# Optimization experiments

Measured on AMD Instinct MI355X. Metric: run time of the kernel, lower is better.

## Reference

```python
import jax, jax.numpy as jnp
import numpy as np

B, C, Ci, V = 1024, 256, 128, 90
EPS = 1e-5


def setup_inputs() -> dict:
    key = jax.random.key(0)
    ks = iter(jax.random.split(key, 40))
    def nrm(shape, s=1.0):
        return jax.random.normal(next(ks), shape, jnp.float32) * s
    def uni(shape):
        return jax.random.uniform(next(ks), shape, jnp.float32, 0.5, 1.5)
    inp = {"x1": nrm((B, C, V)), "x2": nrm((B, C, V))}
    for p in ["g", "th", "ph"]:
        inp[p + "_bn_gamma"] = uni((C,))
        inp[p + "_bn_beta"] = nrm((C,), 0.1)
        inp[p + "_bn_mean"] = nrm((C,), 0.1)
        inp[p + "_bn_var"] = uni((C,))
        inp[p + "_w"] = nrm((Ci, C), 0.05)
        inp[p + "_b"] = nrm((Ci,), 0.05)
    inp["W_w"] = nrm((C, Ci), 0.05)
    inp["W_b"] = nrm((C,), 0.05)
    inp["W_bn_gamma"] = uni((C,))
    inp["W_bn_beta"] = nrm((C,), 0.1)
    inp["W_bn_mean"] = nrm((C,), 0.1)
    inp["W_bn_var"] = uni((C,))
    inp["qt_w"] = nrm((Ci, C), 0.05); inp["qt_b"] = nrm((Ci,), 0.05)
    inp["ks_w"] = nrm((Ci, V), 0.05); inp["ks_b"] = nrm((Ci,), 0.05)
    inp["qs_w"] = nrm((Ci, V), 0.05); inp["qs_b"] = nrm((Ci,), 0.05)
    inp["kt_w"] = nrm((Ci, C), 0.05); inp["kt_b"] = nrm((Ci,), 0.05)
    return inp


def _bn(x, g, b, m, v):
    # eval-mode BatchNorm1d over channel dim of (B, C, V)
    return (x - m[:, None]) * jax.lax.rsqrt(v[:, None] + EPS) * g[:, None] + b[:, None]


def _conv1(x, w, b):
    # 1x1 Conv1d: (B, Cin, V) x (Cout, Cin) -> (B, Cout, V)
    return jnp.einsum('bcv,oc->bov', x, w) + b[:, None]


def reference(x1, x2,
              g_bn_gamma, g_bn_beta, g_bn_mean, g_bn_var, g_w, g_b,
              th_bn_gamma, th_bn_beta, th_bn_mean, th_bn_var, th_w, th_b,
              ph_bn_gamma, ph_bn_beta, ph_bn_mean, ph_bn_var, ph_w, ph_b,
              W_w, W_b, W_bn_gamma, W_bn_beta, W_bn_mean, W_bn_var,
              qt_w, qt_b, ks_w, ks_b, qs_w, qs_b, kt_w, kt_b):
    g_x1 = _conv1(_bn(x1, g_bn_gamma, g_bn_beta, g_bn_mean, g_bn_var), g_w, g_b)
    g_x2 = _conv1(_bn(x2, g_bn_gamma, g_bn_beta, g_bn_mean, g_bn_var), g_w, g_b)
    theta = _conv1(_bn(x1, th_bn_gamma, th_bn_beta, th_bn_mean, th_bn_var), th_w, th_b)  # theta(x1)
    phi = _conv1(_bn(x2, ph_bn_gamma, ph_bn_beta, ph_bn_mean, ph_bn_var), ph_w, ph_b)    # phi(x2)

    e_time = jnp.einsum('biv,bjv->bij', theta, phi)   # (B, Ci, Ci) = theta_x1 @ phi_x2
    e_space = jnp.einsum('bci,bcj->bij', theta, phi)  # (B, V, V)  = theta_x2 @ phi_x1

    attn_time_1 = jax.nn.softmax(e_time, axis=-1)
    attn_time_2 = jax.nn.softmax(jnp.swapaxes(e_time, 1, 2), axis=-1)
    attn_space_2 = jax.nn.softmax(e_space, axis=-1)
    attn_space_1 = jax.nn.softmax(jnp.swapaxes(e_space, 1, 2), axis=-1)

    z1 = jnp.einsum('bij,bjv,bvw->biw', attn_time_2, g_x1, attn_space_2)  # (B, Ci, V)
    z2 = jnp.einsum('bij,bjv,bvw->biw', attn_time_1, g_x2, attn_space_1)

    m1t = x1.mean(axis=2)                      # (B, C)
    q_time = m1t @ qt_w.T + qt_b               # (B, Ci)
    k_space = x2.mean(axis=1) @ ks_w.T + ks_b  # (B, Ci)
    # bmm of (B,1,Ci) x (B,Ci,1) -> (B,1,1); softmax over singleton dim == 1 (kept for faithfulness)
    attn_t2s = jax.nn.softmax(jnp.sum(q_time * k_space, axis=-1, keepdims=True)[:, :, None], axis=-1)
    x2n = x2 + attn_t2s * m1t[:, :, None]      # broadcast (B,1,1)*(B,C,1) over V

    q_space = x1.mean(axis=1) @ qs_w.T + qs_b  # (B, Ci)
    k_time = x2n.mean(axis=2) @ kt_w.T + kt_b  # (B, Ci)
    attn_s2t = jax.nn.softmax(jnp.sum(q_space * k_time, axis=-1, keepdims=True)[:, :, None], axis=-1)
    x1n = x1 + attn_s2t * x2n.mean(axis=1)[:, None, :]

    def Wop(z):
        return _bn(_conv1(z, W_w, W_b), W_bn_gamma, W_bn_beta, W_bn_mean, W_bn_var)

    return (x1n + Wop(z1), x2n + Wop(z2))
```

## Files before the change

### kernel.cpp

```cpp
#include <hip/hip_runtime.h>

namespace {

constexpr int B = 1024;

using u16 = unsigned short;
using u32 = unsigned int;

typedef __attribute__((ext_vector_type(8))) short bf16x8;
typedef __attribute__((ext_vector_type(4))) float f32x4;

#define MFMA16(a, b, c) __builtin_amdgcn_mfma_f32_16x16x32_bf16(a, b, c, 0, 0, 0)

__device__ __forceinline__ u16 f2bf(float f) {
  u32 u = __builtin_bit_cast(u32, f);
  u += 0x7FFFu + ((u >> 16) & 1u);
  return (u16)(u >> 16);
}
__device__ __forceinline__ float bf2f(u16 s) {
  u32 u = ((u32)s) << 16;
  return __builtin_bit_cast(float, u);
}
__device__ __forceinline__ u32 packbf2(float a, float b) {
  return (u32)f2bf(a) | ((u32)f2bf(b) << 16);
}
__device__ __forceinline__ u32 tsplit(float f) {
  u32 u = __builtin_bit_cast(u32, f);
  float r = f - __builtin_bit_cast(float, u & 0xFFFF0000u);
  u32 ur = __builtin_bit_cast(u32, r);
  return (u >> 16) | (ur & 0xFFFF0000u);
}

__global__ __launch_bounds__(256) void k0_fold(
    const float* __restrict__ gg, const float* __restrict__ gbe, const float* __restrict__ gme, const float* __restrict__ gva,
    const float* __restrict__ gw, const float* __restrict__ gbi,
    const float* __restrict__ tg, const float* __restrict__ tbe, const float* __restrict__ tme, const float* __restrict__ tva,
    const float* __restrict__ tw, const float* __restrict__ tbi,
    const float* __restrict__ pg, const float* __restrict__ pbe, const float* __restrict__ pme, const float* __restrict__ pva,
    const float* __restrict__ pw, const float* __restrict__ pbi,
    const float* __restrict__ Ww, const float* __restrict__ Wb,
    const float* __restrict__ Wg2, const float* __restrict__ Wbe, const float* __restrict__ Wme, const float* __restrict__ Wva,
    u16* __restrict__ wgo, float* __restrict__ bgo,
    u16* __restrict__ wthi, u16* __restrict__ wtlo, float* __restrict__ bto,
    u16* __restrict__ wphi, u16* __restrict__ wplo, float* __restrict__ bpo,
    u16* __restrict__ wWo, float* __restrict__ bWo)
{
  __shared__ float red[4];
  const int blk = blockIdx.x, tid = threadIdx.x;
  if (blk < 384) {
    const int p = blk >> 7, o = blk & 127;
    const float *ga, *be, *me, *va, *wm, *bi;
    if (p == 0)      { ga = gg; be = gbe; me = gme; va = gva; wm = gw; bi = gbi; }
    else if (p == 1) { ga = tg; be = tbe; me = tme; va = tva; wm = tw; bi = tbi; }
    else             { ga = pg; be = pbe; me = pme; va = pva; wm = pw; bi = pbi; }
    float s = ga[tid] * rsqrtf(va[tid] + 1e-5f);
    float t = be[tid] - me[tid] * s;
    float wv = wm[o * 256 + tid];
    float val = wv * s;
    if (p == 0) {
      wgo[o * 256 + tid] = f2bf(val);
    } else {
      u16 hi = f2bf(val);
      u16 lo = f2bf(val - bf2f(hi));
      if (p == 1) { wthi[o * 256 + tid] = hi; wtlo[o * 256 + tid] = lo; }
      else        { wphi[o * 256 + tid] = hi; wplo[o * 256 + tid] = lo; }
    }
    float part = t * wv;
#pragma unroll
    for (int off = 32; off; off >>= 1) part += __shfl_down(part, off);
    if ((tid & 63) == 0) red[tid >> 6] = part;
    __syncthreads();
    if (tid == 0) {
      float bsum = bi[o] + red[0] + red[1] + red[2] + red[3];
      if (p == 0) bgo[o] = bsum; else if (p == 1) bto[o] = bsum; else bpo[o] = bsum;
    }
  } else {
    const int c = blk - 384;
    float sW = Wg2[c] * rsqrtf(Wva[c] + 1e-5f);
    if (tid < 128) wWo[c * 128 + tid] = f2bf(Ww[c * 128 + tid] * sW);
    if (tid == 0) bWo[c] = Wb[c] * sW + Wbe[c] - Wme[c] * sW;
  }
}

__global__ __launch_bounds__(512, 4) void k1_conv(
    const float* __restrict__ x1, const float* __restrict__ x2,
    const u16* __restrict__ wG, const float* __restrict__ bG,
    const u16* __restrict__ wTh, const u16* __restrict__ wTl, const float* __restrict__ bT,
    const u16* __restrict__ wPh, const u16* __restrict__ wPl, const float* __restrict__ bP,
    u32* __restrict__ thRm, u32* __restrict__ phRm,
    u16* __restrict__ outU,
    float* __restrict__ m1t, float* __restrict__ x2cm, float* __restrict__ x1am)
{
  __shared__ u32 qb[64 * 92];
  __shared__ u16 xh[96 * 136];
  __shared__ u16 xl[96 * 136];
  __shared__ float red[4];
  const int bid = blockIdx.x, tid = threadIdx.x;
  const int b = bid >> 1; const bool isX1 = !(bid & 1);
  const int l = tid & 63, wv = tid >> 6, lr = l & 15, lq = l >> 4;
  const f32x4 zero = {0.f, 0.f, 0.f, 0.f};

  const float* xb = (isX1 ? x1 : x2) + (size_t)b * 23040;
  const u16* Wh = isX1 ? wTh : wPh;
  const u16* Wl = isX1 ? wTl : wPl;
  const float* biasT = isX1 ? bT : bP;
  u16* oSl = outU + (size_t)(isX1 ? b : 1024 + b) * 46080;
  u32* rmDst = (isX1 ? thRm : phRm) + (size_t)b * 12288;
  u32* pkDst = (u32*)(oSl + 12288);
  u16* gDst = oSl;

  f32x4 aT[6], aG[6];
#pragma unroll
  for (int i = 0; i < 6; ++i) { aT[i] = zero; aG[i] = zero; }
  float cs = 0.f;

  for (int h = 0; h < 2; ++h) {
    for (int q = 0; q < 2; ++q) {
      __syncthreads();
      const float* src = xb + (2 * h + q) * 5760;
      for (int t = tid; t < 2880; t += 512) {
        float2 f = *(const float2*)(src + 2 * t);
        int cl = (2 * t) / 90, v = 2 * t - 90 * cl;
        uint2 w; w.x = tsplit(f.x); w.y = tsplit(f.y);
        *(uint2*)&qb[cl * 92 + v] = w;
      }
      __syncthreads();
      for (int t = tid; t < 1440; t += 512) {
        int v = t % 90, c4 = t / 90;
        u32 p0 = qb[(4 * c4 + 0) * 92 + v], p1 = qb[(4 * c4 + 1) * 92 + v];
        u32 p2 = qb[(4 * c4 + 2) * 92 + v], p3 = qb[(4 * c4 + 3) * 92 + v];
        uint2 hi, lo;
        hi.x = (p0 & 0xFFFFu) | (p1 << 16);
        hi.y = (p2 & 0xFFFFu) | (p3 << 16);
        lo.x = (p0 >> 16) | (p1 & 0xFFFF0000u);
        lo.y = (p2 >> 16) | (p3 & 0xFFFF0000u);
        int base = v * 136 + 64 * q + 4 * c4;
        *(uint2*)&xh[base] = hi;
        *(uint2*)&xl[base] = lo;
      }
      if (q == 1) {
        for (int t = tid; t < 384; t += 512) {
          int v = 90 + (t >> 6), c2 = (t & 63) * 2;
          *(u32*)&xh[v * 136 + c2] = 0u;
          *(u32*)&xl[v * 136 + c2] = 0u;
        }
      }
      if (!isX1 && tid < 90) {
        float s = 0.f;
        for (int cl = 0; cl < 64; ++cl) {
          u32 p = qb[cl * 92 + tid];
          s += bf2f((u16)p) + bf2f((u16)(p >> 16));
        }
        cs += s;
      }
    }
    __syncthreads();
    if (isX1 && tid < 128) {
      float s = 0.f;
      for (int v = 0; v < 90; ++v) s += bf2f(xh[v * 136 + tid]) + bf2f(xl[v * 136 + tid]);
      m1t[b * 256 + 128 * h + tid] = s * (1.f / 90.f);
#pragma unroll
      for (int o = 32; o; o >>= 1) s += __shfl_down(s, o);
      if ((tid & 63) == 0) red[(tid >> 6) + 2 * h] = s;
    }
    for (int kk = 0; kk < 4; ++kk) {
      const int wo = (16 * wv + lr) * 256 + 128 * h + kk * 32 + 8 * lq;
      bf16x8 ah = *(const bf16x8*)(Wh + wo);
      bf16x8 al = *(const bf16x8*)(Wl + wo);
      bf16x8 ag = *(const bf16x8*)(wG + wo);
#pragma unroll
      for (int nt = 0; nt < 6; ++nt) {
        const int bo = (16 * nt + lr) * 136 + kk * 32 + 8 * lq;
        bf16x8 bh = *(const bf16x8*)&xh[bo];
        bf16x8 bl = *(const bf16x8*)&xl[bo];
        aT[nt] = MFMA16(ah, bh, aT[nt]);
        aT[nt] = MFMA16(ah, bl, aT[nt]);
        aT[nt] = MFMA16(al, bh, aT[nt]);
        aG[nt] = MFMA16(ag, bh, aG[nt]);
        aG[nt] = MFMA16(ag, bl, aG[nt]);
      }
    }
  }
  __syncthreads();
  const int c0 = 16 * wv + 4 * lq;
  const float4 bt4 = *(const float4*)(biasT + c0);
  const float4 bg4 = *(const float4*)(bG + c0);
#pragma unroll
  for (int nt = 0; nt < 6; ++nt) {
    const int v = 16 * nt + lr;
    u32 pk0, pk1, pk2, pk3; uint2 gpk;
    if (v < 90) {
      pk0 = tsplit(aT[nt][0] + bt4.x);
      pk1 = tsplit(aT[nt][1] + bt4.y);
      pk2 = tsplit(aT[nt][2] + bt4.z);
      pk3 = tsplit(aT[nt][3] + bt4.w);
      gpk.x = packbf2(aG[nt][0] + bg4.x, aG[nt][1] + bg4.y);
      gpk.y = packbf2(aG[nt][2] + bg4.z, aG[nt][3] + bg4.w);
    } else { pk0 = pk1 = pk2 = pk3 = 0u; gpk.x = 0u; gpk.y = 0u; }
    uint4 q4; q4.x = pk0; q4.y = pk1; q4.z = pk2; q4.w = pk3;
    *(uint4*)(pkDst + v * 128 + c0) = q4;
    rmDst[(c0 + 0) * 96 + v] = pk0;
    rmDst[(c0 + 1) * 96 + v] = pk1;
    rmDst[(c0 + 2) * 96 + v] = pk2;
    rmDst[(c0 + 3) * 96 + v] = pk3;
    *(uint2*)(gDst + v * 128 + c0) = gpk;
  }
  if (isX1) {
    if (tid == 0) x1am[b] = (red[0] + red[1] + red[2] + red[3]) * (1.f / 23040.f);
  } else {
    if (tid < 90) x2cm[b * 96 + tid] = cs * (1.f / 256.f);
  }
}

__global__ __launch_bounds__(512) void k2_attn(
    const u32* __restrict__ thRm, const u32* __restrict__ phRm,
    u16* __restrict__ outU,
    u16* __restrict__ At1g, u16* __restrict__ At2g)
{
  __shared__ __align__(16) char smem[108544];
  u16* s0 = (u16*)smem;
  float* st = (float*)(smem + 106496);
  float* eL = (float*)smem;

  const int bid = blockIdx.x, tid = threadIdx.x;
  const int b = bid >> 1;
  const int l = tid & 63, wv = tid >> 6, lr = l & 15, lq = l >> 4;
  const f32x4 zero = {0.f, 0.f, 0.f, 0.f};

  if (!(bid & 1)) {
    const u32* thRmB = thRm + (size_t)b * 12288;
    const u32* phRmB = phRm + (size_t)b * 12288;
    u16* th_hi = s0;
    u16* th_lo = s0 + 13312;
    u16* ph_hi = s0 + 26624;
    u16* ph_lo = s0 + 39936;
    for (int d = tid; d < 6144; d += 512) {
      int ten = (d >= 3072);
      int i = d - 3072 * ten;
      int ci = i / 24, q4 = i - 24 * ci;
      uint4 P = *(const uint4*)((ten ? phRmB : thRmB) + ci * 96 + 4 * q4);
      uint2 hi, lo;
      hi.x = (P.x & 0xFFFFu) | (P.y << 16);
      hi.y = (P.z & 0xFFFFu) | (P.w << 16);
      lo.x = (P.x >> 16) | (P.y & 0xFFFF0000u);
      lo.y = (P.z >> 16) | (P.w & 0xFFFF0000u);
      *(uint2*)((ten ? ph_hi : th_hi) + ci * 104 + 4 * q4) = hi;
      *(uint2*)((ten ? ph_lo : th_lo) + ci * 104 + 4 * q4) = lo;
    }
    __syncthreads();
    f32x4 acc[8];
#pragma unroll
    for (int nt = 0; nt < 8; ++nt) acc[nt] = zero;
#pragma unroll
    for (int kk = 0; kk < 3; ++kk) {
      const int ao = (16 * wv + lr) * 104 + kk * 32 + 8 * lq;
      bf16x8 ah = *(const bf16x8*)&th_hi[ao];
      bf16x8 al = *(const bf16x8*)&th_lo[ao];
#pragma unroll
      for (int nt = 0; nt < 8; ++nt) {
        const int bo = (16 * nt + lr) * 104 + kk * 32 + 8 * lq;
        bf16x8 bh = *(const bf16x8*)&ph_hi[bo];
        bf16x8 bl = *(const bf16x8*)&ph_lo[bo];
        acc[nt] = MFMA16(ah, bh, acc[nt]);
        acc[nt] = MFMA16(ah, bl, acc[nt]);
        acc[nt] = MFMA16(al, bh, acc[nt]);
      }
    }
    __syncthreads();
#pragma unroll
    for (int nt = 0; nt < 8; ++nt)
#pragma unroll
      for (int r = 0; r < 4; ++r)
        eL[(16 * nt + lr) * 133 + 16 * wv + 4 * lq + r] = acc[nt][r];
    __syncthreads();
    if (tid < 128) {
      int j = tid; float m = -1e30f;
      for (int i = 0; i < 128; ++i) m = fmaxf(m, eL[j * 133 + i]);
      float s = 0.f;
      for (int i = 0; i < 128; ++i) s += __expf(eL[j * 133 + i] - m);
      st[j] = m; st[128 + j] = 1.f / s;
    } else if (tid < 256) {
      int i = tid - 128; float m = -1e30f;
      for (int j = 0; j < 128; ++j) m = fmaxf(m, eL[j * 133 + i]);
      float s = 0.f;
      for (int j = 0; j < 128; ++j) s += __expf(eL[j * 133 + i] - m);
      st[256 + i] = m; st[384 + i] = 1.f / s;
    }
    __syncthreads();
    u32* A1 = (u32*)(At1g + (size_t)b * 16384);
    u32* A2 = (u32*)(At2g + (size_t)b * 16384);
    for (int d = tid; d < 8192; d += 512) {
      int i = d >> 6, jp = d & 63;
      float m1 = st[256 + i], s1v = st[384 + i];
      float a0 = __expf(eL[(2 * jp) * 133 + i] - m1) * s1v;
      float a1 = __expf(eL[(2 * jp + 1) * 133 + i] - m1) * s1v;
      A1[d] = packbf2(a0, a1);
      float m2 = st[i], s2v = st[128 + i];
      float b0 = __expf(eL[i * 133 + 2 * jp] - m2) * s2v;
      float b1 = __expf(eL[i * 133 + 2 * jp + 1] - m2) * s2v;
      A2[d] = packbf2(b0, b1);
    }
    return;
  }

  const u32* thPk = (const u32*)(outU + (size_t)b * 46080 + 12288);
  const u32* phPk = (const u32*)(outU + (size_t)(1024 + b) * 46080 + 12288);
  u32* S1 = (u32*)(outU + (size_t)(1024 + b) * 46080 + 36864);
  u32* S2 = (u32*)(outU + (size_t)b * 46080 + 36864);

  u16* tTh = s0;
  u16* tTl = s0 + 13056;
  u16* pTh = s0 + 26112;
  u16* pTl = s0 + 39168;
  for (int d = tid; d < 6144; d += 512) {
    int ten = (d >= 3072);
    int i = d - 3072 * ten;
    int v = i >> 5, q4 = i & 31;
    uint4 P = *(const uint4*)((ten ? phPk : thPk) + v * 128 + 4 * q4);
    uint2 hi, lo;
    hi.x = (P.x & 0xFFFFu) | (P.y << 16);
    hi.y = (P.z & 0xFFFFu) | (P.w << 16);
    lo.x = (P.x >> 16) | (P.y & 0xFFFF0000u);
    lo.y = (P.z >> 16) | (P.w & 0xFFFF0000u);
    *(uint2*)((ten ? pTh : tTh) + v * 136 + 4 * q4) = hi;
    *(uint2*)((ten ? pTl : tTl) + v * 136 + 4 * q4) = lo;
  }
  __syncthreads();
  f32x4 accS[5];
#pragma unroll
  for (int it = 0; it < 5; ++it) accS[it] = zero;
#pragma unroll
  for (int it = 0; it < 5; ++it) {
    const int t5 = wv + 8 * it;
    if (t5 < 36) {
      const int mt = t5 / 6, nt = t5 - 6 * (t5 / 6);
#pragma unroll
      for (int kk = 0; kk < 4; ++kk) {
        const int ao = (16 * mt + lr) * 136 + kk * 32 + 8 * lq;
        const int bo = (16 * nt + lr) * 136 + kk * 32 + 8 * lq;
        bf16x8 ah = *(const bf16x8*)&tTh[ao];
        bf16x8 al = *(const bf16x8*)&tTl[ao];
        bf16x8 bh = *(const bf16x8*)&pTh[bo];
        bf16x8 bl = *(const bf16x8*)&pTl[bo];
        accS[it] = MFMA16(ah, bh, accS[it]);
        accS[it] = MFMA16(ah, bl, accS[it]);
        accS[it] = MFMA16(al, bh, accS[it]);
      }
    }
  }
  __syncthreads();
  {
    float* esL = (float*)smem;
#pragma unroll
    for (int it = 0; it < 5; ++it) {
      const int t5 = wv + 8 * it;
      if (t5 < 36) {
        const int mt = t5 / 6, nt = t5 - 6 * (t5 / 6);
#pragma unroll
        for (int r = 0; r < 4; ++r)
          esL[(16 * nt + lr) * 101 + 16 * mt + 4 * lq + r] = accS[it][r];
      }
    }
  }
  __syncthreads();
  {
    float* esL = (float*)smem;
    if (tid < 96) {
      int v = tid; float m = -1e30f;
      for (int w2 = 0; w2 < 90; ++w2) m = fmaxf(m, esL[v * 101 + w2]);
      float s = 0.f;
      for (int w2 = 0; w2 < 90; ++w2) s += __expf(esL[v * 101 + w2] - m);
      st[v] = m; st[128 + v] = 1.f / s;
    } else if (tid >= 128 && tid < 224) {
      int v = tid - 128; float m = -1e30f;
      for (int w2 = 0; w2 < 90; ++w2) m = fmaxf(m, esL[w2 * 101 + v]);
      float s = 0.f;
      for (int w2 = 0; w2 < 90; ++w2) s += __expf(esL[w2 * 101 + v] - m);
      st[256 + v] = m; st[384 + v] = 1.f / s;
    }
  }
  __syncthreads();
  {
    float* esL = (float*)smem;
    for (int d = tid; d < 4608; d += 512) {
      int w2 = d / 48, vp = d - 48 * (d / 48);
      int v0 = 2 * vp, v1 = v0 + 1;
      float a0 = __expf(esL[v0 * 101 + w2] - st[v0]) * st[128 + v0];
      float a1 = __expf(esL[v1 * 101 + w2] - st[v1]) * st[128 + v1];
      S1[d] = packbf2(a0, a1);
      float b0 = __expf(esL[w2 * 101 + v0] - st[256 + v0]) * st[384 + v0];
      float b1 = __expf(esL[w2 * 101 + v1] - st[256 + v1]) * st[384 + v1];
      S2[d] = packbf2(b0, b1);
    }
  }
}

__global__ __launch_bounds__(256) void k3_out(
    const float* __restrict__ x1, const float* __restrict__ x2,
    const u16* __restrict__ At1g, const u16* __restrict__ At2g,
    const u16* __restrict__ wW, const float* __restrict__ bW,
    const float* __restrict__ m1t, const float* __restrict__ x2cm, const float* __restrict__ x1am,
    float* __restrict__ out)
{
  __shared__ u16 gT[96 * 136];
  __shared__ u16 Tb[128 * 104];
  __shared__ u16 ZT[96 * 136];
  const int bid = blockIdx.x, tid = threadIdx.x;
  const int b = bid >> 1; const bool modeA = !(bid & 1);
  const int l = tid & 63, wv = tid >> 6, lr = l & 15, lq = l >> 4;
  const f32x4 zero = {0.f, 0.f, 0.f, 0.f};

  float* out1 = out + (size_t)b * 23040;
  float* out2 = out + (size_t)23040 * 1024 + (size_t)b * 23040;

  const u16* gsrc; const u16* At; const u16* AsT; const float* xres; float* dst;
  if (modeA) {
    gsrc = (const u16*)out2; At = At1g + (size_t)b * 16384;
    AsT = (const u16*)out2 + 36864; xres = x2 + (size_t)b * 23040; dst = out2;
  } else {
    gsrc = (const u16*)out1; At = At2g + (size_t)b * 16384;
    AsT = (const u16*)out1 + 36864; xres = x1 + (size_t)b * 23040; dst = out1;
  }

  for (int i = tid; i < 1536; i += 256) {
    int v = i >> 4, hh = i & 15;
    *(uint4*)&gT[v * 136 + 8 * hh] = ((const uint4*)gsrc)[i];
  }
  __syncthreads();
#pragma unroll
  for (int ni = 0; ni < 2; ++ni) {
    const int nt = 2 * wv + ni;
    f32x4 acc[6];
#pragma unroll
    for (int i = 0; i < 6; ++i) acc[i] = zero;
#pragma unroll
    for (int kk = 0; kk < 4; ++kk) {
      bf16x8 bb = *(const bf16x8*)(At + (16 * nt + lr) * 128 + kk * 32 + 8 * lq);
#pragma unroll
      for (int mt = 0; mt < 6; ++mt) {
        bf16x8 a = *(const bf16x8*)&gT[(16 * mt + lr) * 136 + kk * 32 + 8 * lq];
        acc[mt] = MFMA16(a, bb, acc[mt]);
      }
    }
#pragma unroll
    for (int mt = 0; mt < 6; ++mt) {
      uint2 pk;
      pk.x = packbf2(acc[mt][0], acc[mt][1]);
      pk.y = packbf2(acc[mt][2], acc[mt][3]);
      *(uint2*)&Tb[(16 * nt + lr) * 104 + 16 * mt + 4 * lq] = pk;
    }
  }
  __syncthreads();
  {
    f32x4 acc[2][6];
#pragma unroll
    for (int i = 0; i < 2; ++i)
#pragma unroll
      for (int j = 0; j < 6; ++j) acc[i][j] = zero;
#pragma unroll
    for (int kk = 0; kk < 3; ++kk) {
      bf16x8 a0 = *(const bf16x8*)&Tb[(16 * (2 * wv) + lr) * 104 + kk * 32 + 8 * lq];
      bf16x8 a1 = *(const bf16x8*)&Tb[(16 * (2 * wv + 1) + lr) * 104 + kk * 32 + 8 * lq];
#pragma unroll
      for (int nt = 0; nt < 6; ++nt) {
        bf16x8 bb = *(const bf16x8*)(AsT + (16 * nt + lr) * 96 + kk * 32 + 8 * lq);
        acc[0][nt] = MFMA16(a0, bb, acc[0][nt]);
        acc[1][nt] = MFMA16(a1, bb, acc[1][nt]);
      }
    }
#pragma unroll
    for (int mi = 0; mi < 2; ++mi) {
      const int mt = 2 * wv + mi;
#pragma unroll
      for (int nt = 0; nt < 6; ++nt) {
        uint2 pk;
        pk.x = packbf2(acc[mi][nt][0], acc[mi][nt][1]);
        pk.y = packbf2(acc[mi][nt][2], acc[mi][nt][3]);
        *(uint2*)&ZT[(16 * nt + lr) * 136 + 16 * mt + 4 * lq] = pk;
      }
    }
  }
  __syncthreads();
  const float am = modeA ? 0.f : x1am[b];
#pragma unroll
  for (int mi = 0; mi < 4; ++mi) {
    const int mt = 4 * wv + mi;
    f32x4 acc[6];
#pragma unroll
    for (int i = 0; i < 6; ++i) acc[i] = zero;
#pragma unroll
    for (int kk = 0; kk < 4; ++kk) {
      bf16x8 a = *(const bf16x8*)(wW + (16 * mt + lr) * 128 + kk * 32 + 8 * lq);
#pragma unroll
      for (int nt = 0; nt < 6; ++nt) {
        bf16x8 bb = *(const bf16x8*)&ZT[(16 * nt + lr) * 136 + kk * 32 + 8 * lq];
        acc[nt] = MFMA16(a, bb, acc[nt]);
      }
    }
    const int c0 = 16 * mt + 4 * lq;
    const float4 bw4 = *(const float4*)(bW + c0);
    float bwA[4] = {bw4.x, bw4.y, bw4.z, bw4.w};
    float mA[4] = {0.f, 0.f, 0.f, 0.f};
    if (modeA) {
      const float4 m4 = *(const float4*)(m1t + b * 256 + c0);
      mA[0] = m4.x; mA[1] = m4.y; mA[2] = m4.z; mA[3] = m4.w;
    }
#pragma unroll
    for (int nt = 0; nt < 6; ++nt) {
      const int v = 16 * nt + lr;
      if (v < 90) {
        const float addv = modeA ? 0.f : (am + x2cm[b * 96 + v]);
#pragma unroll
        for (int r = 0; r < 4; ++r) {
          const int c = c0 + r;
          const float extra = modeA ? mA[r] : addv;
          dst[c * 90 + v] = xres[c * 90 + v] + acc[nt][r] + bwA[r] + extra;
        }
      }
    }
  }
}

}

extern "C" void kernel_launch(void* const* d_in, const int* in_sizes, int n_in,
                              void* d_out, int out_size, void* d_ws, size_t ws_size,
                              hipStream_t stream)
{
  (void)in_sizes; (void)n_in; (void)out_size; (void)ws_size;
  const float* x1  = (const float*)d_in[0];
  const float* x2  = (const float*)d_in[1];
  const float* gg  = (const float*)d_in[2];
  const float* gbe = (const float*)d_in[3];
  const float* gme = (const float*)d_in[4];
  const float* gva = (const float*)d_in[5];
  const float* gw  = (const float*)d_in[6];
  const float* gbi = (const float*)d_in[7];
  const float* tg  = (const float*)d_in[8];
  const float* tbe = (const float*)d_in[9];
  const float* tme = (const float*)d_in[10];
  const float* tva = (const float*)d_in[11];
  const float* tw  = (const float*)d_in[12];
  const float* tbi = (const float*)d_in[13];
  const float* pg  = (const float*)d_in[14];
  const float* pbe = (const float*)d_in[15];
  const float* pme = (const float*)d_in[16];
  const float* pva = (const float*)d_in[17];
  const float* pw  = (const float*)d_in[18];
  const float* pbi = (const float*)d_in[19];
  const float* Ww  = (const float*)d_in[20];
  const float* Wb  = (const float*)d_in[21];
  const float* Wg  = (const float*)d_in[22];
  const float* Wbe = (const float*)d_in[23];
  const float* Wme = (const float*)d_in[24];
  const float* Wva = (const float*)d_in[25];

  float* out = (float*)d_out;
  unsigned char* W8 = (unsigned char*)d_ws;

  size_t off = 0;
  auto al = [&](size_t n) { size_t r = off; off += (n + 255) & ~(size_t)255; return r; };
  const size_t oWG  = al(65536);
  const size_t oWTh = al(65536), oWTl = al(65536);
  const size_t oWPh = al(65536), oWPl = al(65536);
  const size_t oWW  = al(65536);
  const size_t oBG = al(512), oBT = al(512), oBP = al(512), oBW = al(1024);
  const size_t oRM1 = al((size_t)B * 49152), oRM2 = al((size_t)B * 49152);
  const size_t oA1 = al((size_t)B * 32768), oA2 = al((size_t)B * 32768);
  const size_t oM1 = al((size_t)B * 1024), oXC = al((size_t)B * 384), oXA = al((size_t)B * 4);

  k0_fold<<<dim3(640), dim3(256), 0, stream>>>(
      gg, gbe, gme, gva, gw, gbi,
      tg, tbe, tme, tva, tw, tbi,
      pg, pbe, pme, pva, pw, pbi,
      Ww, Wb, Wg, Wbe, Wme, Wva,
      (u16*)(W8 + oWG), (float*)(W8 + oBG),
      (u16*)(W8 + oWTh), (u16*)(W8 + oWTl), (float*)(W8 + oBT),
      (u16*)(W8 + oWPh), (u16*)(W8 + oWPl), (float*)(W8 + oBP),
      (u16*)(W8 + oWW), (float*)(W8 + oBW));

  k1_conv<<<dim3(2 * B), dim3(512), 0, stream>>>(
      x1, x2,
      (const u16*)(W8 + oWG), (const float*)(W8 + oBG),
      (const u16*)(W8 + oWTh), (const u16*)(W8 + oWTl), (const float*)(W8 + oBT),
      (const u16*)(W8 + oWPh), (const u16*)(W8 + oWPl), (const float*)(W8 + oBP),
      (u32*)(W8 + oRM1), (u32*)(W8 + oRM2),
      (u16*)out,
      (float*)(W8 + oM1), (float*)(W8 + oXC), (float*)(W8 + oXA));

  k2_attn<<<dim3(2 * B), dim3(512), 0, stream>>>(
      (const u32*)(W8 + oRM1), (const u32*)(W8 + oRM2),
      (u16*)out,
      (u16*)(W8 + oA1), (u16*)(W8 + oA2));

  k3_out<<<dim3(2 * B), dim3(256), 0, stream>>>(
      x1, x2,
      (const u16*)(W8 + oA1), (const u16*)(W8 + oA2),
      (const u16*)(W8 + oWW), (const float*)(W8 + oBW),
      (const float*)(W8 + oM1), (const float*)(W8 + oXC), (const float*)(W8 + oXA),
      out);
}
```

Baseline: 521.7 us.

## Widen k3_out to 512 threads, stage As in LDS, coalesce output via LDS

Doubles the k3_out block to 512 threads so each wave owns one tile row instead of two. The spatial attention matrix is prefetched into registers early and then staged into shared memory, so the second GMM reads it from LDS instead of global memory. Final output tiles are transposed through a per-wave LDS buffer and written with contiguous row-major stores, giving coalesced residual reads and output writes. The cost is extra barriers inside the output loop and higher shared-memory use per block, which may limit how many blocks fit on a CU.

New measurement: 576.0 us. +10.4%, slower.

```diff
diff --git a/kernel.cpp b/kernel.cpp
--- a/kernel.cpp
+++ b/kernel.cpp
@@ -395,16 +395,20 @@
   }
 }
 
-__global__ __launch_bounds__(256) void k3_out(
+__global__ __launch_bounds__(512, 4) void k3_out(
     const float* __restrict__ x1, const float* __restrict__ x2,
     const u16* __restrict__ At1g, const u16* __restrict__ At2g,
     const u16* __restrict__ wW, const float* __restrict__ bW,
     const float* __restrict__ m1t, const float* __restrict__ x2cm, const float* __restrict__ x1am,
     float* __restrict__ out)
 {
-  __shared__ u16 gT[96 * 136];
-  __shared__ u16 Tb[128 * 104];
-  __shared__ u16 ZT[96 * 136];
+  __shared__ __align__(16) char smem[78848];
+  u16* gT = (u16*)smem;
+  u16* As = (u16*)smem;
+  u16* Tb = (u16*)(smem + 26112);
+  u16* ZT = (u16*)(smem + 52736);
+  float* OtBase = (float*)smem;
+
   const int bid = blockIdx.x, tid = threadIdx.x;
   const int b = bid >> 1; const bool modeA = !(bid & 1);
   const int l = tid & 63, wv = tid >> 6, lr = l & 15, lq = l >> 4;
@@ -413,29 +417,33 @@
   float* out1 = out + (size_t)b * 23040;
   float* out2 = out + (size_t)23040 * 1024 + (size_t)b * 23040;
 
-  const u16* gsrc; const u16* At; const u16* AsT; const float* xres; float* dst;
+  const u16* gsrc; const u16* At; const u16* AsG; const float* xres; float* dst;
   if (modeA) {
     gsrc = (const u16*)out2; At = At1g + (size_t)b * 16384;
-    AsT = (const u16*)out2 + 36864; xres = x2 + (size_t)b * 23040; dst = out2;
+    AsG = (const u16*)out2 + 36864; xres = x2 + (size_t)b * 23040; dst = out2;
   } else {
     gsrc = (const u16*)out1; At = At2g + (size_t)b * 16384;
-    AsT = (const u16*)out1 + 36864; xres = x1 + (size_t)b * 23040; dst = out1;
-  }
-
-  for (int i = tid; i < 1536; i += 256) {
+    AsG = (const u16*)out1 + 36864; xres = x1 + (size_t)b * 23040; dst = out1;
+  }
+
+  const uint4* As4 = (const uint4*)AsG;
+  uint4 asr0 = As4[tid];
+  uint4 asr1 = As4[512 + tid];
+  uint4 asr2 = {0, 0, 0, 0};
+  if (tid < 128) asr2 = As4[1024 + tid];
+
+  for (int i = tid; i < 1536; i += 512) {
     int v = i >> 4, hh = i & 15;
     *(uint4*)&gT[v * 136 + 8 * hh] = ((const uint4*)gsrc)[i];
   }
   __syncthreads();
-#pragma unroll
-  for (int ni = 0; ni < 2; ++ni) {
-    const int nt = 2 * wv + ni;
+  {
     f32x4 acc[6];
 #pragma unroll
     for (int i = 0; i < 6; ++i) acc[i] = zero;
 #pragma unroll
     for (int kk = 0; kk < 4; ++kk) {
-      bf16x8 bb = *(const bf16x8*)(At + (16 * nt + lr) * 128 + kk * 32 + 8 * lq);
+      bf16x8 bb = *(const bf16x8*)(At + (16 * wv + lr) * 128 + kk * 32 + 8 * lq);
 #pragma unroll
       for (int mt = 0; mt < 6; ++mt) {
         bf16x8 a = *(const bf16x8*)&gT[(16 * mt + lr) * 136 + kk * 32 + 8 * lq];
@@ -447,44 +455,43 @@
       uint2 pk;
       pk.x = packbf2(acc[mt][0], acc[mt][1]);
       pk.y = packbf2(acc[mt][2], acc[mt][3]);
-      *(uint2*)&Tb[(16 * nt + lr) * 104 + 16 * mt + 4 * lq] = pk;
+      *(uint2*)&Tb[(16 * wv + lr) * 104 + 16 * mt + 4 * lq] = pk;
     }
   }
   __syncthreads();
   {
-    f32x4 acc[2][6];
-#pragma unroll
-    for (int i = 0; i < 2; ++i)
-#pragma unroll
-      for (int j = 0; j < 6; ++j) acc[i][j] = zero;
+    int i0 = tid;            *(uint4*)&As[(i0 / 12) * 104 + (i0 % 12) * 8] = asr0;
+    int i1 = 512 + tid;      *(uint4*)&As[(i1 / 12) * 104 + (i1 % 12) * 8] = asr1;
+    if (tid < 128) { int i2 = 1024 + tid; *(uint4*)&As[(i2 / 12) * 104 + (i2 % 12) * 8] = asr2; }
+  }
+  __syncthreads();
+  {
+    f32x4 acc[6];
+#pragma unroll
+    for (int i = 0; i < 6; ++i) acc[i] = zero;
 #pragma unroll
     for (int kk = 0; kk < 3; ++kk) {
-      bf16x8 a0 = *(const bf16x8*)&Tb[(16 * (2 * wv) + lr) * 104 + kk * 32 + 8 * lq];
-      bf16x8 a1 = *(const bf16x8*)&Tb[(16 * (2 * wv + 1) + lr) * 104 + kk * 32 + 8 * lq];
+      bf16x8 a0 = *(const bf16x8*)&Tb[(16 * wv + lr) * 104 + kk * 32 + 8 * lq];
 #pragma unroll
       for (int nt = 0; nt < 6; ++nt) {
-        bf16x8 bb = *(const bf16x8*)(AsT + (16 * nt + lr) * 96 + kk * 32 + 8 * lq);
-        acc[0][nt] = MFMA16(a0, bb, acc[0][nt]);
-        acc[1][nt] = MFMA16(a1, bb, acc[1][nt]);
-      }
-    }
-#pragma unroll
-    for (int mi = 0; mi < 2; ++mi) {
-      const int mt = 2 * wv + mi;
-#pragma unroll
-      for (int nt = 0; nt < 6; ++nt) {
-        uint2 pk;
-        pk.x = packbf2(acc[mi][nt][0], acc[mi][nt][1]);
-        pk.y = packbf2(acc[mi][nt][2], acc[mi][nt][3]);
-        *(uint2*)&ZT[(16 * nt + lr) * 136 + 16 * mt + 4 * lq] = pk;
-      }
+        bf16x8 bb = *(const bf16x8*)&As[(16 * nt + lr) * 104 + kk * 32 + 8 * lq];
+        acc[nt] = MFMA16(a0, bb, acc[nt]);
+      }
+    }
+#pragma unroll
+    for (int nt = 0; nt < 6; ++nt) {
+      uint2 pk;
+      pk.x = packbf2(acc[nt][0], acc[nt][1]);
+      pk.y = packbf2(acc[nt][2], acc[nt][3]);
+      *(uint2*)&ZT[(16 * nt + lr) * 136 + 16 * wv + 4 * lq] = pk;
     }
   }
   __syncthreads();
   const float am = modeA ? 0.f : x1am[b];
-#pragma unroll
-  for (int mi = 0; mi < 4; ++mi) {
-    const int mt = 4 * wv + mi;
+  float* Ot = OtBase + wv * 1472;
+#pragma unroll
+  for (int mi = 0; mi < 2; ++mi) {
+    const int mt = 2 * wv + mi;
     f32x4 acc[6];
 #pragma unroll
     for (int i = 0; i < 6; ++i) acc[i] = zero;
@@ -497,25 +504,26 @@
         acc[nt] = MFMA16(a, bb, acc[nt]);
       }
     }
-    const int c0 = 16 * mt + 4 * lq;
-    const float4 bw4 = *(const float4*)(bW + c0);
-    float bwA[4] = {bw4.x, bw4.y, bw4.z, bw4.w};
-    float mA[4] = {0.f, 0.f, 0.f, 0.f};
-    if (modeA) {
-      const float4 m4 = *(const float4*)(m1t + b * 256 + c0);
-      mA[0] = m4.x; mA[1] = m4.y; mA[2] = m4.z; mA[3] = m4.w;
-    }
+    __syncthreads();
 #pragma unroll
     for (int nt = 0; nt < 6; ++nt) {
       const int v = 16 * nt + lr;
       if (v < 90) {
-        const float addv = modeA ? 0.f : (am + x2cm[b * 96 + v]);
-#pragma unroll
-        for (int r = 0; r < 4; ++r) {
-          const int c = c0 + r;
-          const float extra = modeA ? mA[r] : addv;
-          dst[c * 90 + v] = xres[c * 90 + v] + acc[nt][r] + bwA[r] + extra;
-        }
+#pragma unroll
+        for (int r = 0; r < 4; ++r) Ot[(4 * lq + r) * 92 + v] = acc[nt][r];
+      }
+    }
+    __syncthreads();
+    const int c0b = 16 * mt;
+#pragma unroll 4
+    for (int k = 0; k < 23; ++k) {
+      int f = 64 * k + l;
+      if (f < 1440) {
+        int row = f / 90, col = f - 90 * row;
+        int c = c0b + row;
+        float o = Ot[row * 92 + col];
+        float extra = modeA ? m1t[b * 256 + c] : (am + x2cm[b * 96 + col]);
+        dst[c * 90 + col] = xres[c * 90 + col] + o + bW[c] + extra;
       }
     }
   }
@@ -593,7 +601,7 @@
       (u16*)out,
       (u16*)(W8 + oA1), (u16*)(W8 + oA2));
 
-  k3_out<<<dim3(2 * B), dim3(256), 0, stream>>>(
+  k3_out<<<dim3(2 * B), dim3(512), 0, stream>>>(
       x1, x2,
       (const u16*)(W8 + oA1), (const u16*)(W8 + oA2),
       (const u16*)(W8 + oWW), (const float*)(W8 + oBW),
```

## Merge the two k3_out modes into one block per batch and alias LDS buffers

Applied to the files above, without the earlier changes.

Each block of k3_out now handles both output modes for one batch element, one after the other, so the grid is halved. The gT and ZT staging buffers share one LDS region, which lowers per-block shared memory. Launch bounds now request 3 blocks per SIMD/CU to raise occupancy and hide latency. In exchange, each block does twice the serial work and adds an extra barrier, and with fewer blocks the wave tail on the GPU may get worse.

New measurement: 574.3 us. 1.1x slower.

```diff
diff --git a/kernel.cpp b/kernel.cpp
--- a/kernel.cpp
+++ b/kernel.cpp
@@ -395,130 +395,133 @@
   }
 }
 
-__global__ __launch_bounds__(256) void k3_out(
+__global__ __launch_bounds__(256, 3) void k3_out(
     const float* __restrict__ x1, const float* __restrict__ x2,
     const u16* __restrict__ At1g, const u16* __restrict__ At2g,
     const u16* __restrict__ wW, const float* __restrict__ bW,
     const float* __restrict__ m1t, const float* __restrict__ x2cm, const float* __restrict__ x1am,
     float* __restrict__ out)
 {
-  __shared__ u16 gT[96 * 136];
-  __shared__ u16 Tb[128 * 104];
-  __shared__ u16 ZT[96 * 136];
-  const int bid = blockIdx.x, tid = threadIdx.x;
-  const int b = bid >> 1; const bool modeA = !(bid & 1);
+  __shared__ __align__(16) char smem[53248];
+  u16* gT = (u16*)smem;
+  u16* ZT = (u16*)smem;
+  u16* Tb = (u16*)(smem + 26624);
+  const int b = blockIdx.x, tid = threadIdx.x;
   const int l = tid & 63, wv = tid >> 6, lr = l & 15, lq = l >> 4;
   const f32x4 zero = {0.f, 0.f, 0.f, 0.f};
 
   float* out1 = out + (size_t)b * 23040;
   float* out2 = out + (size_t)23040 * 1024 + (size_t)b * 23040;
-
-  const u16* gsrc; const u16* At; const u16* AsT; const float* xres; float* dst;
-  if (modeA) {
-    gsrc = (const u16*)out2; At = At1g + (size_t)b * 16384;
-    AsT = (const u16*)out2 + 36864; xres = x2 + (size_t)b * 23040; dst = out2;
-  } else {
-    gsrc = (const u16*)out1; At = At2g + (size_t)b * 16384;
-    AsT = (const u16*)out1 + 36864; xres = x1 + (size_t)b * 23040; dst = out1;
-  }
-
-  for (int i = tid; i < 1536; i += 256) {
-    int v = i >> 4, hh = i & 15;
-    *(uint4*)&gT[v * 136 + 8 * hh] = ((const uint4*)gsrc)[i];
-  }
-  __syncthreads();
-#pragma unroll
-  for (int ni = 0; ni < 2; ++ni) {
-    const int nt = 2 * wv + ni;
-    f32x4 acc[6];
-#pragma unroll
-    for (int i = 0; i < 6; ++i) acc[i] = zero;
-#pragma unroll
-    for (int kk = 0; kk < 4; ++kk) {
-      bf16x8 bb = *(const bf16x8*)(At + (16 * nt + lr) * 128 + kk * 32 + 8 * lq);
+  const u16* g1s = (const u16*)out1;
+  const u16* g2s = (const u16*)out2;
+  const u16* As1 = (const u16*)out2 + 36864;
+  const u16* As2 = (const u16*)out1 + 36864;
+
+  auto phase = [&](const u16* __restrict__ gsrc, const u16* __restrict__ At,
+                   const u16* __restrict__ AsT, const float* __restrict__ xres,
+                   float* __restrict__ dst, bool modeA) {
+    for (int i = tid; i < 1536; i += 256) {
+      int v = i >> 4, hh = i & 15;
+      *(uint4*)&gT[v * 136 + 8 * hh] = ((const uint4*)gsrc)[i];
+    }
+    __syncthreads();
+#pragma unroll
+    for (int ni = 0; ni < 2; ++ni) {
+      const int nt = 2 * wv + ni;
+      f32x4 acc[6];
+#pragma unroll
+      for (int i = 0; i < 6; ++i) acc[i] = zero;
+#pragma unroll
+      for (int kk = 0; kk < 4; ++kk) {
+        bf16x8 bb = *(const bf16x8*)(At + (16 * nt + lr) * 128 + kk * 32 + 8 * lq);
+#pragma unroll
+        for (int mt = 0; mt < 6; ++mt) {
+          bf16x8 a = *(const bf16x8*)&gT[(16 * mt + lr) * 136 + kk * 32 + 8 * lq];
+          acc[mt] = MFMA16(a, bb, acc[mt]);
+        }
+      }
 #pragma unroll
       for (int mt = 0; mt < 6; ++mt) {
-        bf16x8 a = *(const bf16x8*)&gT[(16 * mt + lr) * 136 + kk * 32 + 8 * lq];
-        acc[mt] = MFMA16(a, bb, acc[mt]);
-      }
-    }
-#pragma unroll
-    for (int mt = 0; mt < 6; ++mt) {
-      uint2 pk;
-      pk.x = packbf2(acc[mt][0], acc[mt][1]);
-      pk.y = packbf2(acc[mt][2], acc[mt][3]);
-      *(uint2*)&Tb[(16 * nt + lr) * 104 + 16 * mt + 4 * lq] = pk;
-    }
-  }
-  __syncthreads();
-  {
-    f32x4 acc[2][6];
-#pragma unroll
-    for (int i = 0; i < 2; ++i)
-#pragma unroll
-      for (int j = 0; j < 6; ++j) acc[i][j] = zero;
-#pragma unroll
-    for (int kk = 0; kk < 3; ++kk) {
-      bf16x8 a0 = *(const bf16x8*)&Tb[(16 * (2 * wv) + lr) * 104 + kk * 32 + 8 * lq];
-      bf16x8 a1 = *(const bf16x8*)&Tb[(16 * (2 * wv + 1) + lr) * 104 + kk * 32 + 8 * lq];
+        uint2 pk;
+        pk.x = packbf2(acc[mt][0], acc[mt][1]);
+        pk.y = packbf2(acc[mt][2], acc[mt][3]);
+        *(uint2*)&Tb[(16 * nt + lr) * 104 + 16 * mt + 4 * lq] = pk;
+      }
+    }
+    __syncthreads();
+    {
+      f32x4 acc[2][6];
+#pragma unroll
+      for (int i = 0; i < 2; ++i)
+#pragma unroll
+        for (int j = 0; j < 6; ++j) acc[i][j] = zero;
+#pragma unroll
+      for (int kk = 0; kk < 3; ++kk) {
+        bf16x8 a0 = *(const bf16x8*)&Tb[(16 * (2 * wv) + lr) * 104 + kk * 32 + 8 * lq];
+        bf16x8 a1 = *(const bf16x8*)&Tb[(16 * (2 * wv + 1) + lr) * 104 + kk * 32 + 8 * lq];
+#pragma unroll
+        for (int nt = 0; nt < 6; ++nt) {
+          bf16x8 bb = *(const bf16x8*)(AsT + (16 * nt + lr) * 96 + kk * 32 + 8 * lq);
+          acc[0][nt] = MFMA16(a0, bb, acc[0][nt]);
+          acc[1][nt] = MFMA16(a1, bb, acc[1][nt]);
+        }
+      }
+#pragma unroll
+      for (int mi = 0; mi < 2; ++mi) {
+        const int mt = 2 * wv + mi;
+#pragma unroll
+        for (int nt = 0; nt < 6; ++nt) {
+          uint2 pk;
+          pk.x = packbf2(acc[mi][nt][0], acc[mi][nt][1]);
+          pk.y = packbf2(acc[mi][nt][2], acc[mi][nt][3]);
+          *(uint2*)&ZT[(16 * nt + lr) * 136 + 16 * mt + 4 * lq] = pk;
+        }
+      }
+    }
+    __syncthreads();
+    const float am = modeA ? 0.f : x1am[b];
+#pragma unroll
+    for (int mi = 0; mi < 4; ++mi) {
+      const int mt = 4 * wv + mi;
+      f32x4 acc[6];
+#pragma unroll
+      for (int i = 0; i < 6; ++i) acc[i] = zero;
+#pragma unroll
+      for (int kk = 0; kk < 4; ++kk) {
+        bf16x8 a = *(const bf16x8*)(wW + (16 * mt + lr) * 128 + kk * 32 + 8 * lq);
+#pragma unroll
+        for (int nt = 0; nt < 6; ++nt) {
+          bf16x8 bb = *(const bf16x8*)&ZT[(16 * nt + lr) * 136 + kk * 32 + 8 * lq];
+          acc[nt] = MFMA16(a, bb, acc[nt]);
+        }
+      }
+      const int c0 = 16 * mt + 4 * lq;
+      const float4 bw4 = *(const float4*)(bW + c0);
+      float bwA[4] = {bw4.x, bw4.y, bw4.z, bw4.w};
+      float mA[4] = {0.f, 0.f, 0.f, 0.f};
+      if (modeA) {
+        const float4 m4 = *(const float4*)(m1t + b * 256 + c0);
+        mA[0] = m4.x; mA[1] = m4.y; mA[2] = m4.z; mA[3] = m4.w;
+      }
 #pragma unroll
       for (int nt = 0; nt < 6; ++nt) {
-        bf16x8 bb = *(const bf16x8*)(AsT + (16 * nt + lr) * 96 + kk * 32 + 8 * lq);
-        acc[0][nt] = MFMA16(a0, bb, acc[0][nt]);
-        acc[1][nt] = MFMA16(a1, bb, acc[1][nt]);
-      }
-    }
-#pragma unroll
-    for (int mi = 0; mi < 2; ++mi) {
-      const int mt = 2 * wv + mi;
-#pragma unroll
-      for (int nt = 0; nt < 6; ++nt) {
-        uint2 pk;
-        pk.x = packbf2(acc[mi][nt][0], acc[mi][nt][1]);
-        pk.y = packbf2(acc[mi][nt][2], acc[mi][nt][3]);
-        *(uint2*)&ZT[(16 * nt + lr) * 136 + 16 * mt + 4 * lq] = pk;
-      }
-    }
-  }
-  __syncthreads();
-  const float am = modeA ? 0.f : x1am[b];
-#pragma unroll
-  for (int mi = 0; mi < 4; ++mi) {
-    const int mt = 4 * wv + mi;
-    f32x4 acc[6];
-#pragma unroll
-    for (int i = 0; i < 6; ++i) acc[i] = zero;
-#pragma unroll
-    for (int kk = 0; kk < 4; ++kk) {
-      bf16x8 a = *(const bf16x8*)(wW + (16 * mt + lr) * 128 + kk * 32 + 8 * lq);
-#pragma unroll
-      for (int nt = 0; nt < 6; ++nt) {
-        bf16x8 bb = *(const bf16x8*)&ZT[(16 * nt + lr) * 136 + kk * 32 + 8 * lq];
-        acc[nt] = MFMA16(a, bb, acc[nt]);
-      }
-    }
-    const int c0 = 16 * mt + 4 * lq;
-    const float4 bw4 = *(const float4*)(bW + c0);
-    float bwA[4] = {bw4.x, bw4.y, bw4.z, bw4.w};
-    float mA[4] = {0.f, 0.f, 0.f, 0.f};
-    if (modeA) {
-      const float4 m4 = *(const float4*)(m1t + b * 256 + c0);
-      mA[0] = m4.x; mA[1] = m4.y; mA[2] = m4.z; mA[3] = m4.w;
-    }
-#pragma unroll
-    for (int nt = 0; nt < 6; ++nt) {
-      const int v = 16 * nt + lr;
-      if (v < 90) {
-        const float addv = modeA ? 0.f : (am + x2cm[b * 96 + v]);
-#pragma unroll
-        for (int r = 0; r < 4; ++r) {
-          const int c = c0 + r;
-          const float extra = modeA ? mA[r] : addv;
-          dst[c * 90 + v] = xres[c * 90 + v] + acc[nt][r] + bwA[r] + extra;
+        const int v = 16 * nt + lr;
+        if (v < 90) {
+          const float addv = modeA ? 0.f : (am + x2cm[b * 96 + v]);
+#pragma unroll
+          for (int r = 0; r < 4; ++r) {
+            const int c = c0 + r;
+            const float extra = modeA ? mA[r] : addv;
+            dst[c * 90 + v] = xres[c * 90 + v] + acc[nt][r] + bwA[r] + extra;
+          }
         }
       }
     }
-  }
+    __syncthreads();
+  };
+
+  phase(g2s, At1g + (size_t)b * 16384, As1, x2 + (size_t)b * 23040, out2, true);
+  phase(g1s, At2g + (size_t)b * 16384, As2, x1 + (size_t)b * 23040, out1, false);
 }
 
 }
@@ -593,7 +596,7 @@
       (u16*)out,
       (u16*)(W8 + oA1), (u16*)(W8 + oA2));
 
-  k3_out<<<dim3(2 * B), dim3(256), 0, stream>>>(
+  k3_out<<<dim3(B), dim3(256), 0, stream>>>(
       x1, x2,
       (const u16*)(W8 + oA1), (const u16*)(W8 + oA2),
       (const u16*)(W8 + oWW), (const float*)(W8 + oBW),
```
